# Kernel tuning notes

Hardware: AMD Instinct MI355X
Metric: run time of the kernel (lower is better)

Reference implementation:

```python
import jax, jax.numpy as jnp
import numpy as np

B, S, D, H, FF = 2, 2048, 1024, 16, 4096
HD = D // H          # head dim = 64
ROT = HD // 2        # rotary dim = dim/(num_heads*2) = 32 (partial rotation)
EPS = 1e-5


def setup_inputs() -> dict:
    key = jax.random.key(0)
    ks = jax.random.split(key, 16)
    std = 0.02
    return {
        "x": jax.random.normal(ks[0], (B, S, D), jnp.float32),
        "mask": jnp.ones((B, 1, 1, S), jnp.int32),
        "wq": jax.random.normal(ks[1], (D, D), jnp.float32) * std,
        "bq": jnp.zeros((D,), jnp.float32),
        "wk": jax.random.normal(ks[2], (D, D), jnp.float32) * std,
        "bk": jnp.zeros((D,), jnp.float32),
        "wv": jax.random.normal(ks[3], (D, D), jnp.float32) * std,
        "bv": jnp.zeros((D,), jnp.float32),
        "wo": jax.random.normal(ks[4], (D, D), jnp.float32) * std,
        "bo": jnp.zeros((D,), jnp.float32),
        "ln1_w": jnp.ones((D,), jnp.float32),
        "ln1_b": jnp.zeros((D,), jnp.float32),
        "ln2_w": jnp.ones((D,), jnp.float32),
        "ln2_b": jnp.zeros((D,), jnp.float32),
        "w1": jax.random.normal(ks[5], (D, FF), jnp.float32) * std,
        "b1": jnp.zeros((FF,), jnp.float32),
        "w2": jax.random.normal(ks[6], (FF, D), jnp.float32) * std,
        "b2": jnp.zeros((D,), jnp.float32),
    }


def _layernorm(x, w, b):
    mu = jnp.mean(x, axis=-1, keepdims=True)
    var = jnp.mean(jnp.square(x - mu), axis=-1, keepdims=True)
    return (x - mu) * jax.lax.rsqrt(var + EPS) * w + b


def _rope(t):
    # t: [B, H, S, HD]; rotate first ROT features, interleaved (GPT-J) pairing
    inv_freq = 1.0 / (10000.0 ** (jnp.arange(0, ROT, 2, dtype=jnp.float32) / ROT))
    ang = jnp.arange(S, dtype=jnp.float32)[:, None] * inv_freq      # [S, ROT//2]
    ang = jnp.repeat(ang, 2, axis=-1)                               # [S, ROT]
    cos, sin = jnp.cos(ang), jnp.sin(ang)
    t_rot, t_pass = t[..., :ROT], t[..., ROT:]
    pr = t_rot.reshape(*t_rot.shape[:-1], ROT // 2, 2)
    rot = jnp.stack([-pr[..., 1], pr[..., 0]], axis=-1).reshape(t_rot.shape)
    return jnp.concatenate([t_rot * cos + rot * sin, t_pass], axis=-1)


def reference(x, mask, wq, bq, wk, bk, wv, bv, wo, bo,
              ln1_w, ln1_b, ln2_w, ln2_b, w1, b1, w2, b2):
    res = x
    h = _layernorm(x, ln1_w, ln1_b)
    q = (h @ wq + bq).reshape(B, S, H, HD).transpose(0, 2, 1, 3)
    k = (h @ wk + bk).reshape(B, S, H, HD).transpose(0, 2, 1, 3)
    v = (h @ wv + bv).reshape(B, S, H, HD).transpose(0, 2, 1, 3)
    q, k = _rope(q), _rope(k)
    score = jnp.einsum('bhqd,bhkd->bhqk', q, k) * (1.0 / np.sqrt(HD))
    score = jnp.where(mask == 0, jnp.float32(-1e9), score)
    attn = jax.nn.softmax(score, axis=-1)
    out = jnp.einsum('bhqk,bhkd->bhqd', attn, v)
    out = out.transpose(0, 2, 1, 3).reshape(B, S, D) @ wo + bo
    x = res + out
    res = x
    h = _layernorm(x, ln2_w, ln2_b)
    h = jax.nn.gelu(h @ w1 + b1, approximate=False) @ w2 + b2
    return res + h
```

## Files before the change

kernel.cpp:

```cpp
#include <hip/hip_runtime.h>
#include <cstdint>
#include <cstddef>


typedef __bf16 bf16;
typedef __bf16 bf16x2 __attribute__((ext_vector_type(2)));
typedef __bf16 bf16x4v __attribute__((ext_vector_type(4)));
typedef __bf16 bf16x8 __attribute__((ext_vector_type(8)));
typedef float  f32x4  __attribute__((ext_vector_type(4)));

#define NB 2
#define NS 2048
#define ND 1024
#define NH 16
#define NHD 64
#define NFF 4096
#define NM (NB*NS)
#define QKSCALE 0.18033688011112042f

typedef uint32_t __attribute__((address_space(1))) gu32_t;
typedef uint32_t __attribute__((address_space(3))) lu32_t;
__device__ __forceinline__ void async_copy16(void* lds, const void* g) {
  __builtin_amdgcn_global_load_lds((gu32_t*)g, (lu32_t*)lds, 16, 0, 0);
}

__device__ __forceinline__ bf16x4v tr_read16(const void* p) {
  typedef const __attribute__((address_space(3))) unsigned char* lp;
  bf16x4v d;
  asm volatile("ds_read_b64_tr_b16 %0, %1" : "=v"(d) : "v"((lp)p));
  return d;
}

__device__ __forceinline__ float gelu_f(float x) {
  return 0.5f * x * (1.0f + erff(x * 0.70710678118654752f));
}

__global__ __launch_bounds__(256) void transpose_all(
    const float* __restrict__ wq, const float* __restrict__ wk,
    const float* __restrict__ wv, const float* __restrict__ wo,
    const float* __restrict__ w1, const float* __restrict__ w2,
    bf16* __restrict__ wqt, bf16* __restrict__ wkt, bf16* __restrict__ wvt,
    bf16* __restrict__ wot, bf16* __restrict__ w1t, bf16* __restrict__ w2t) {
  __shared__ float t[32][33];
  int flat = blockIdx.x;
  const float* W; bf16* Wt; long bx, by; int K, N;
  if (flat < 4096) {
    int which = flat >> 10, r = flat & 1023;
    const float* Ws[4] = {wq, wk, wv, wo};
    bf16* Wts[4] = {wqt, wkt, wvt, wot};
    W = Ws[which]; Wt = Wts[which]; bx = r & 31; by = r >> 5; K = ND; N = ND;
  } else if (flat < 8192) {
    int r = flat - 4096;
    W = w1; Wt = w1t; bx = r & 127; by = r >> 7; K = ND; N = NFF;
  } else {
    int r = flat - 8192;
    W = w2; Wt = w2t; bx = r & 31; by = r >> 5; K = NFF; N = ND;
  }
  int tx = threadIdx.x, ty = threadIdx.y;
#pragma unroll
  for (int r = 0; r < 4; ++r)
    t[ty + r*8][tx] = W[(by*32 + ty + r*8) * (long)N + bx*32 + tx];
  __syncthreads();
#pragma unroll
  for (int r = 0; r < 4; ++r)
    Wt[(bx*32 + ty + r*8) * (long)K + by*32 + tx] = (bf16)t[tx][ty + r*8];
}

__global__ __launch_bounds__(256) void smallfuse_kernel(
    const float* __restrict__ a, const float* __restrict__ b,
    const float* __restrict__ c, float* __restrict__ o,
    const int* __restrict__ mask, float* __restrict__ m01f,
    bf16* __restrict__ m01b, float2* __restrict__ rtab) {
  int blk = blockIdx.x;
  int t = threadIdx.x;
  if (blk < 12) {
    int i = blk * 256 + t;
    o[i] = (i < ND) ? a[i] : ((i < 2*ND) ? b[i - ND] : c[i - 2*ND]);
  } else if (blk < 28) {
    int i = (blk - 12) * 256 + t;
    float v = mask[i] ? 1.0f : 0.0f;
    m01f[i] = v;
    m01b[i] = (bf16)v;
  } else {
    int idx = (blk - 28) * 256 + t;
    int s = idx >> 4, i = idx & 15;
    float ang = (float)s * exp2f(-(float)i * (13.287712379549449f / 16.0f));
    float sn, cs;
    sincosf(ang, &sn, &cs);
    rtab[idx] = make_float2(cs, sn);
  }
}

__global__ __launch_bounds__(256) void ln_kernel(
    const float* __restrict__ x, const float* __restrict__ w,
    const float* __restrict__ b, bf16* __restrict__ out) {
  long row = blockIdx.x;
  int t = threadIdx.x;
  float4 v = ((const float4*)(x + row*ND))[t];
  float s  = v.x + v.y + v.z + v.w;
  float sq = v.x*v.x + v.y*v.y + v.z*v.z + v.w*v.w;
#pragma unroll
  for (int m = 1; m <= 32; m <<= 1) { s += __shfl_xor(s, m); sq += __shfl_xor(sq, m); }
  __shared__ float ss[4], ssq[4];
  if ((t & 63) == 0) { ss[t>>6] = s; ssq[t>>6] = sq; }
  __syncthreads();
  s  = ss[0] + ss[1] + ss[2] + ss[3];
  sq = ssq[0] + ssq[1] + ssq[2] + ssq[3];
  float mu = s * (1.0f/ND);
  float rs = rsqrtf(sq * (1.0f/ND) - mu*mu + 1e-5f);
  float4 wv = ((const float4*)w)[t];
  float4 bv = ((const float4*)b)[t];
  bf16x4v o;
  o[0] = (bf16)((v.x-mu)*rs*wv.x + bv.x);
  o[1] = (bf16)((v.y-mu)*rs*wv.y + bv.y);
  o[2] = (bf16)((v.z-mu)*rs*wv.z + bv.z);
  o[3] = (bf16)((v.w-mu)*rs*wv.w + bv.w);
  *(bf16x4v*)(out + row*ND + t*4) = o;
}

template<int EPI>
__global__ __launch_bounds__(512, 2) void gemm256_kernel(
    const bf16* __restrict__ A, const bf16* __restrict__ Bt,
    const float* __restrict__ bias, void* __restrict__ Cout,
    const float2* __restrict__ rtab, const float* __restrict__ m01f,
    int M, int N, int K) {
  __shared__ __align__(16) bf16 Alds[4][256*32];
  __shared__ __align__(16) bf16 Blds[4][256*32];
  const int tid = threadIdx.x, lane = tid & 63, w = tid >> 6;
  const int fr = lane & 15, kg = lane >> 4;
  const int wr = w >> 2, wc = w & 3;
  const int swb = (kg ^ ((fr >> 1) & 3)) << 4;

  const int gx = gridDim.x;
  int lin = blockIdx.y * gx + blockIdx.x;
  int nwg = gx * gridDim.y;
  int swz = (lin & 7) * (nwg >> 3) + (lin >> 3);
  const long am0 = (long)(swz / gx) * 256;
  const long bn0 = (long)(swz % gx) * 256;

  const f32x4 fzero = {0.f, 0.f, 0.f, 0.f};
  f32x4 acc[8][4];
#pragma unroll
  for (int m = 0; m < 8; ++m)
#pragma unroll
    for (int n = 0; n < 4; ++n) acc[m][n] = fzero;

  auto stage = [&](int kt, int bufi) {
#pragma unroll
    for (int i = 0; i < 2; ++i) {
      int s = i*512 + tid;
      int r = s >> 2, c = (s & 3) ^ ((s >> 3) & 3);
      async_copy16((char*)&Alds[bufi][0] + i*8192 + w*1024,
                   &A[(am0 + r)*K + kt + c*8]);
      async_copy16((char*)&Blds[bufi][0] + i*8192 + w*1024,
                   &Bt[(bn0 + r)*K + kt + c*8]);
    }
  };

  const int nk = K >> 5;
  stage(0, 0);
  stage(32, 1);
  asm volatile("s_waitcnt vmcnt(4)" ::: "memory");
  __builtin_amdgcn_s_barrier();
  __builtin_amdgcn_sched_barrier(0);

  for (int t = 0; t < nk; ++t) {
    const int cur = t & 3;
    if (t + 2 < nk) stage((t + 2) * 32, (t + 2) & 3);
    const char* Ab = (const char*)&Alds[cur][0];
    const char* Bb = (const char*)&Blds[cur][0];
    bf16x8 af[4], bfv[4];
#pragma unroll
    for (int n = 0; n < 4; ++n) bfv[n] = *(const bf16x8*)(Bb + (wc*64 + n*16 + fr)*64 + swb);
#pragma unroll
    for (int m = 0; m < 4; ++m) af[m]  = *(const bf16x8*)(Ab + (wr*128 + m*16 + fr)*64 + swb);
    asm volatile("s_waitcnt lgkmcnt(0)" ::: "memory");
    __builtin_amdgcn_sched_barrier(0);
    __builtin_amdgcn_s_setprio(1);
#pragma unroll
    for (int m = 0; m < 4; ++m)
#pragma unroll
      for (int n = 0; n < 4; ++n)
        acc[m][n] = __builtin_amdgcn_mfma_f32_16x16x32_bf16(af[m], bfv[n], acc[m][n], 0, 0, 0);
    __builtin_amdgcn_s_setprio(0);
    __builtin_amdgcn_s_barrier();
#pragma unroll
    for (int m = 0; m < 4; ++m) af[m] = *(const bf16x8*)(Ab + (wr*128 + (m+4)*16 + fr)*64 + swb);
    asm volatile("s_waitcnt lgkmcnt(0)" ::: "memory");
    __builtin_amdgcn_sched_barrier(0);
    __builtin_amdgcn_s_setprio(1);
#pragma unroll
    for (int m = 0; m < 4; ++m)
#pragma unroll
      for (int n = 0; n < 4; ++n)
        acc[m+4][n] = __builtin_amdgcn_mfma_f32_16x16x32_bf16(af[m], bfv[n], acc[m+4][n], 0, 0, 0);
    __builtin_amdgcn_s_setprio(0);
    if (t + 2 < nk) { asm volatile("s_waitcnt vmcnt(4)" ::: "memory"); }
    else            { asm volatile("s_waitcnt vmcnt(0)" ::: "memory"); }
    __builtin_amdgcn_s_barrier();
    __builtin_amdgcn_sched_barrier(0);
  }

  const int rbase = kg * 4;
  const int region = (int)(bn0 >> 10);
#pragma unroll
  for (int m = 0; m < 8; ++m) {
#pragma unroll
    for (int n = 0; n < 4; ++n) {
      long col = bn0 + wc*64 + n*16 + fr;
      float bia = bias[col];
#pragma unroll
      for (int j = 0; j < 4; ++j) {
        long row = am0 + wr*128 + m*16 + rbase + j;
        float val = acc[m][n][j] + bia;
        if (EPI == 1) {
          ((bf16*)Cout)[row * N + col] = (bf16)gelu_f(val);
        } else {
          if (region <= 1) {
            float pval = __shfl_xor(val, 1);
            if (n < 2) {
              float2 cs = rtab[((row & (NS-1)) << 4) | ((n*16 + fr) >> 1)];
              val = (fr & 1) ? val*cs.x + pval*cs.y : val*cs.x - pval*cs.y;
            }
            if (region == 0) val *= QKSCALE;
          } else {
            val *= m01f[row];
          }
          ((bf16*)Cout)[(long)region * (NM*(long)ND) + row * ND + (col & 1023)] = (bf16)val;
        }
      }
    }
  }
}

__global__ __launch_bounds__(512, 1) void gemm128x8_kernel(
    const bf16* __restrict__ A, const bf16* __restrict__ Bt,
    const float* __restrict__ bias, const float* __restrict__ res,
    float* __restrict__ Cout, int M, int N, int K) {
  __shared__ __align__(16) bf16 Alds[4][128*64];
  __shared__ __align__(16) bf16 Blds[4][128*64];
  const int tid = threadIdx.x, lane = tid & 63, w = tid >> 6;
  const int fr = lane & 15, kg = lane >> 4;
  const int wr = w >> 1, wc = w & 1;

  const int gx = gridDim.x;
  int lin = blockIdx.y * gx + blockIdx.x;
  int nwg = gx * gridDim.y;
  int swz = (lin & 7) * (nwg >> 3) + (lin >> 3);
  const long am0 = (long)(swz / gx) * 128;
  const long bn0 = (long)(swz % gx) * 128;

  const f32x4 fzero = {0.f, 0.f, 0.f, 0.f};
  f32x4 acc[2][4];
#pragma unroll
  for (int m = 0; m < 2; ++m)
#pragma unroll
    for (int n = 0; n < 4; ++n) acc[m][n] = fzero;

  auto stage = [&](int kt, int bufi) {
#pragma unroll
    for (int i = 0; i < 2; ++i) {
      int s = i*512 + tid;
      int r = s >> 3, c = (s & 7) ^ (r & 7);
      async_copy16((char*)&Alds[bufi][0] + i*8192 + w*1024,
                   &A[(am0 + r)*K + kt + c*8]);
      async_copy16((char*)&Blds[bufi][0] + i*8192 + w*1024,
                   &Bt[(bn0 + r)*K + kt + c*8]);
    }
  };

  const int nk = K >> 6;
  stage(0, 0);
  stage(64, 1);
  asm volatile("s_waitcnt vmcnt(4)" ::: "memory");
  __builtin_amdgcn_s_barrier();
  __builtin_amdgcn_sched_barrier(0);

  for (int t = 0; t < nk; ++t) {
    const int cur = t & 3;
    if (t + 2 < nk) stage((t + 2) * 64, (t + 2) & 3);
    const char* Ab = (const char*)&Alds[cur][0];
    const char* Bb = (const char*)&Blds[cur][0];
    bf16x8 af[2][2], bfv[2][4];
#pragma unroll
    for (int kk = 0; kk < 2; ++kk) {
#pragma unroll
      for (int m = 0; m < 2; ++m) {
        int r = wr*32 + m*16 + fr;
        af[kk][m] = *(const bf16x8*)(Ab + r*128 + (((kk*4 + kg) ^ (r & 7)) << 4));
      }
#pragma unroll
      for (int n = 0; n < 4; ++n) {
        int r = wc*64 + n*16 + fr;
        bfv[kk][n] = *(const bf16x8*)(Bb + r*128 + (((kk*4 + kg) ^ (r & 7)) << 4));
      }
    }
    asm volatile("s_waitcnt lgkmcnt(0)" ::: "memory");
    __builtin_amdgcn_sched_barrier(0);
    __builtin_amdgcn_s_setprio(1);
#pragma unroll
    for (int kk = 0; kk < 2; ++kk)
#pragma unroll
      for (int m = 0; m < 2; ++m)
#pragma unroll
        for (int n = 0; n < 4; ++n)
          acc[m][n] = __builtin_amdgcn_mfma_f32_16x16x32_bf16(af[kk][m], bfv[kk][n], acc[m][n], 0, 0, 0);
    __builtin_amdgcn_s_setprio(0);
    if (t + 2 < nk) { asm volatile("s_waitcnt vmcnt(4)" ::: "memory"); }
    else            { asm volatile("s_waitcnt vmcnt(0)" ::: "memory"); }
    __builtin_amdgcn_s_barrier();
    __builtin_amdgcn_sched_barrier(0);
  }

  const int rbase = kg * 4;
#pragma unroll
  for (int m = 0; m < 2; ++m) {
#pragma unroll
    for (int n = 0; n < 4; ++n) {
      long col = bn0 + wc*64 + n*16 + fr;
      float bia = bias[col];
#pragma unroll
      for (int j = 0; j < 4; ++j) {
        long row = am0 + wr*32 + m*16 + rbase + j;
        Cout[row * N + col] = acc[m][n][j] + bia + res[row * N + col];
      }
    }
  }
}

__global__ __launch_bounds__(256) void attn_kernel(
    const bf16* __restrict__ q, const bf16* __restrict__ k,
    const bf16* __restrict__ v, const bf16* __restrict__ m01b,
    bf16* __restrict__ out) {
  int lin = blockIdx.y * 32 + blockIdx.x;
  int swz = (lin & 7) * 128 + (lin >> 3);
  const int qt = swz & 31;
  const int b = swz >> 9, h = (swz >> 5) & 15;
  const int tid = threadIdx.x, lane = tid & 63, w = tid >> 6;
  const int fr = lane & 15, kg = lane >> 4;
  const int k8 = kg * 8;
  const int frl = fr & 3, frh = fr >> 2;

  __shared__ __align__(16) bf16 Klds[2][64*64];
  __shared__ __align__(16) bf16 Vlds[2][64*64];

  const long qrow = (long)qt*64 + w*16 + fr;
  const bf16* qbase = q + ((long)b*NS + qrow)*ND + h*NHD;
  bf16x8 qf[2];
  qf[0] = *(const bf16x8*)(qbase + k8);
  qf[1] = *(const bf16x8*)(qbase + 32 + k8);

  const bf16* kbase = k + (long)b*NS*ND + h*NHD;
  const bf16* vbase = v + (long)b*NS*ND + h*NHD;
  const bf16* mbase = m01b + (long)b*NS;

  auto stageK = [&](int kt, int bufi) {
#pragma unroll
    for (int i = 0; i < 2; ++i) {
      int slot = i*256 + tid;
      int row = slot >> 3, c = slot & 7;
      int csrc = c ^ (row & 7) ^ (((row >> 3) & 1) << 2);
      async_copy16((char*)&Klds[bufi][0] + i*4096 + w*1024,
                   kbase + ((long)kt*64 + row)*ND + csrc*8);
    }
  };
  auto stageV = [&](int kt, int bufi) {
#pragma unroll
    for (int i = 0; i < 2; ++i) {
      int kr = i*32 + (tid >> 5)*4 + ((tid & 7) >> 1);
      int dc = ((tid >> 3) & 3)*16 + (tid & 1)*8;
      async_copy16((char*)&Vlds[bufi][0] + i*4096 + w*1024,
                   vbase + ((long)kt*64 + kr)*ND + dc);
    }
  };

  const f32x4 fzero = {0.f, 0.f, 0.f, 0.f};
  f32x4 oacc[4], oaccL = fzero;
#pragma unroll
  for (int n = 0; n < 4; ++n) oacc[n] = fzero;

  stageK(0, 0);
  stageV(0, 0);
  asm volatile("s_waitcnt vmcnt(0)" ::: "memory");
  __builtin_amdgcn_s_barrier();
  __builtin_amdgcn_sched_barrier(0);

  const int NT = NS / 64;
  for (int kt = 0; kt < NT; ++kt) {
    const int cur = kt & 1;
    if (kt + 1 < NT) { stageK(kt + 1, cur ^ 1); stageV(kt + 1, cur ^ 1); }
    bf16x8 vbm[2];
    vbm[0] = *(const bf16x8*)(mbase + kt*64 + k8);
    vbm[1] = *(const bf16x8*)(mbase + kt*64 + 32 + k8);
    const char* Kb = (const char*)&Klds[cur][0];
    const char* Vb = (const char*)&Vlds[cur][0];

    f32x4 sacc[4];
#pragma unroll
    for (int n = 0; n < 4; ++n) sacc[n] = fzero;
#pragma unroll
    for (int n = 0; n < 4; ++n) {
      int r = (frh << 3) + ((n & 1) << 2) + frl + ((n >> 1) << 5);
      int swzr = (r & 7) ^ (((r >> 3) & 1) << 2);
#pragma unroll
      for (int kk = 0; kk < 2; ++kk) {
        bf16x8 kf = *(const bf16x8*)(Kb + r*128 + ((((kk << 2) | kg) ^ swzr) << 4));
        sacc[n] = __builtin_amdgcn_mfma_f32_16x16x32_bf16(kf, qf[kk], sacc[n], 0, 0, 0);
      }
    }

    float p[4][4];
#pragma unroll
    for (int n = 0; n < 4; ++n) {
      p[n][0] = exp2f(sacc[n][0]);
      p[n][1] = exp2f(sacc[n][1]);
      p[n][2] = exp2f(sacc[n][2]);
      p[n][3] = exp2f(sacc[n][3]);
    }

    bf16x8 paf[2];
#pragma unroll
    for (int n = 0; n < 4; ++n) {
#pragma unroll
      for (int j = 0; j < 4; ++j)
        paf[n >> 1][((n & 1) << 2) + j] = (bf16)p[n][j];
    }

    oaccL = __builtin_amdgcn_mfma_f32_16x16x32_bf16(paf[0], vbm[0], oaccL, 0, 0, 0);
    oaccL = __builtin_amdgcn_mfma_f32_16x16x32_bf16(paf[1], vbm[1], oaccL, 0, 0, 0);

#pragma unroll
    for (int kk = 0; kk < 2; ++kk) {
      bf16x4v t0[4], t1[4];
#pragma unroll
      for (int n2 = 0; n2 < 4; ++n2) {
        t0[n2] = tr_read16(Vb + (((kk*8 + 0)*4 + n2)*128 + kg*1024 + fr*8));
        t1[n2] = tr_read16(Vb + (((kk*8 + 1)*4 + n2)*128 + kg*1024 + fr*8));
      }
      asm volatile("s_waitcnt lgkmcnt(0)" ::: "memory");
      __builtin_amdgcn_sched_barrier(0);
#pragma unroll
      for (int n2 = 0; n2 < 4; ++n2) {
        bf16x8 vb8 = __builtin_shufflevector(t0[n2], t1[n2], 0, 1, 2, 3, 4, 5, 6, 7);
        oacc[n2] = __builtin_amdgcn_mfma_f32_16x16x32_bf16(paf[kk], vb8, oacc[n2], 0, 0, 0);
      }
    }

    asm volatile("s_waitcnt vmcnt(0)" ::: "memory");
    __builtin_amdgcn_s_barrier();
    __builtin_amdgcn_sched_barrier(0);
  }

#pragma unroll
  for (int j = 0; j < 4; ++j) {
    float inv = 1.0f / oaccL[j];
    long orow = (long)qt*64 + w*16 + kg*4 + j;
    bf16* ob = out + ((long)b*NS + orow)*ND + h*NHD;
#pragma unroll
    for (int n2 = 0; n2 < 4; ++n2) ob[n2*16 + fr] = (bf16)(oacc[n2][j] * inv);
  }
}

extern "C" void kernel_launch(void* const* d_in, const int* in_sizes, int n_in,
                              void* d_out, int out_size, void* d_ws, size_t ws_size,
                              hipStream_t stream) {
  const float* x    = (const float*)d_in[0];
  const int*   mask = (const int*)d_in[1];
  const float* wq   = (const float*)d_in[2];
  const float* bq   = (const float*)d_in[3];
  const float* wk   = (const float*)d_in[4];
  const float* bk   = (const float*)d_in[5];
  const float* wv   = (const float*)d_in[6];
  const float* bv   = (const float*)d_in[7];
  const float* wo   = (const float*)d_in[8];
  const float* bo   = (const float*)d_in[9];
  const float* ln1w = (const float*)d_in[10];
  const float* ln1b = (const float*)d_in[11];
  const float* ln2w = (const float*)d_in[12];
  const float* ln2b = (const float*)d_in[13];
  const float* w1   = (const float*)d_in[14];
  const float* b1   = (const float*)d_in[15];
  const float* w2   = (const float*)d_in[16];
  const float* b2   = (const float*)d_in[17];
  float* out = (float*)d_out;

  char* ws = (char*)d_ws;
  const size_t MB = 1024ull * 1024ull;
  bf16* wqt = (bf16*)(ws + 0*MB);
  bf16* wkt = (bf16*)(ws + 2*MB);
  bf16* wvt = (bf16*)(ws + 4*MB);
  bf16* wot = (bf16*)(ws + 6*MB);
  bf16* w1t = (bf16*)(ws + 8*MB);
  bf16* w2t = (bf16*)(ws + 16*MB);
  bf16* h1   = (bf16*)(ws + 24*MB);
  bf16* qb   = (bf16*)(ws + 32*MB);
  bf16* kb   = (bf16*)(ws + 40*MB);
  bf16* vb   = (bf16*)(ws + 48*MB);
  bf16* attn = h1;
  bf16* f1   = (bf16*)(ws + 24*MB);
  float* y1  = (float*)(ws + 56*MB);
  bf16* h2   = (bf16*)(ws + 72*MB);
  float* bcat = (float*)(ws + 80*MB);
  float* m01f = (float*)(ws + 80*MB + 16*1024);
  bf16*  m01b = (bf16*) (ws + 80*MB + 32*1024);
  float2* rtab = (float2*)(ws + 80*MB + 48*1024);
  (void)in_sizes; (void)n_in; (void)out_size; (void)ws_size;

  transpose_all<<<12288, dim3(32, 8), 0, stream>>>(wq, wk, wv, wo, w1, w2,
                                                   wqt, wkt, wvt, wot, w1t, w2t);
  smallfuse_kernel<<<156, 256, 0, stream>>>(bq, bk, bv, bcat, mask, m01f, m01b, rtab);

  ln_kernel<<<NM, 256, 0, stream>>>(x, ln1w, ln1b, h1);

  gemm256_kernel<3><<<dim3(12, 16), 512, 0, stream>>>(h1, wqt, bcat, qb,
                                                      rtab, m01f, NM, 3*ND, ND);
  attn_kernel<<<dim3(NS/64, NB*NH), 256, 0, stream>>>(qb, kb, vb, m01b, attn);

  gemm128x8_kernel<<<dim3(8, 32), 512, 0, stream>>>(attn, wot, bo, x, y1,
                                                    NM, ND, ND);
  ln_kernel<<<NM, 256, 0, stream>>>(y1, ln2w, ln2b, h2);
  gemm256_kernel<1><<<dim3(16, 16), 512, 0, stream>>>(h2, w1t, b1, f1,
                                                      nullptr, nullptr, NM, NFF, ND);
  gemm128x8_kernel<<<dim3(8, 32), 512, 0, stream>>>(f1, w2t, b2, y1, out,
                                                    NM, ND, NFF);
}
```

Before: 297.0 us.

## Merge prep kernels, pre-transpose V, triple-buffer attention with 128-row tiles

Folds the weight transpose, small setup work and the first layernorm into one prep kernel, removing two launches. The QKV GEMM epilogue now writes V transposed per head so attention can read V fragments with plain vector LDS loads instead of transpose reads. The attention kernel moves to 512 threads covering 128 query rows, triple-buffers K/V in LDS with a two-tile prefetch, and stages the mask in LDS. The price is more LDS per block, scattered strided writes of V in the GEMM epilogue, and a large merged prep grid.

```diff
diff --git a/kernel.cpp b/kernel.cpp
--- a/kernel.cpp
+++ b/kernel.cpp
@@ -24,70 +24,87 @@
   __builtin_amdgcn_global_load_lds((gu32_t*)g, (lu32_t*)lds, 16, 0, 0);
 }
 
-__device__ __forceinline__ bf16x4v tr_read16(const void* p) {
-  typedef const __attribute__((address_space(3))) unsigned char* lp;
-  bf16x4v d;
-  asm volatile("ds_read_b64_tr_b16 %0, %1" : "=v"(d) : "v"((lp)p));
-  return d;
-}
-
 __device__ __forceinline__ float gelu_f(float x) {
   return 0.5f * x * (1.0f + erff(x * 0.70710678118654752f));
 }
 
-__global__ __launch_bounds__(256) void transpose_all(
+__global__ __launch_bounds__(256) void prep_kernel(
     const float* __restrict__ wq, const float* __restrict__ wk,
     const float* __restrict__ wv, const float* __restrict__ wo,
     const float* __restrict__ w1, const float* __restrict__ w2,
     bf16* __restrict__ wqt, bf16* __restrict__ wkt, bf16* __restrict__ wvt,
-    bf16* __restrict__ wot, bf16* __restrict__ w1t, bf16* __restrict__ w2t) {
-  __shared__ float t[32][33];
+    bf16* __restrict__ wot, bf16* __restrict__ w1t, bf16* __restrict__ w2t,
+    const float* __restrict__ bq, const float* __restrict__ bk,
+    const float* __restrict__ bv, float* __restrict__ bcat,
+    const int* __restrict__ mask, float* __restrict__ m01f,
+    bf16* __restrict__ m01b, float2* __restrict__ rtab,
+    const float* __restrict__ x, const float* __restrict__ ln1w,
+    const float* __restrict__ ln1b, bf16* __restrict__ h1) {
   int flat = blockIdx.x;
-  const float* W; bf16* Wt; long bx, by; int K, N;
-  if (flat < 4096) {
-    int which = flat >> 10, r = flat & 1023;
-    const float* Ws[4] = {wq, wk, wv, wo};
-    bf16* Wts[4] = {wqt, wkt, wvt, wot};
-    W = Ws[which]; Wt = Wts[which]; bx = r & 31; by = r >> 5; K = ND; N = ND;
-  } else if (flat < 8192) {
-    int r = flat - 4096;
-    W = w1; Wt = w1t; bx = r & 127; by = r >> 7; K = ND; N = NFF;
+  int t = threadIdx.x;
+  if (flat < 12288) {
+    __shared__ float tile[32][33];
+    const float* W; bf16* Wt; long bx, by; int K, N;
+    if (flat < 4096) {
+      int which = flat >> 10, r = flat & 1023;
+      const float* Ws[4] = {wq, wk, wv, wo};
+      bf16* Wts[4] = {wqt, wkt, wvt, wot};
+      W = Ws[which]; Wt = Wts[which]; bx = r & 31; by = r >> 5; K = ND; N = ND;
+    } else if (flat < 8192) {
+      int r = flat - 4096;
+      W = w1; Wt = w1t; bx = r & 127; by = r >> 7; K = ND; N = NFF;
+    } else {
+      int r = flat - 8192;
+      W = w2; Wt = w2t; bx = r & 31; by = r >> 5; K = NFF; N = ND;
+    }
+    int tx = t & 31, ty = t >> 5;
+#pragma unroll
+    for (int r = 0; r < 4; ++r)
+      tile[ty + r*8][tx] = W[(by*32 + ty + r*8) * (long)N + bx*32 + tx];
+    __syncthreads();
+#pragma unroll
+    for (int r = 0; r < 4; ++r)
+      Wt[(bx*32 + ty + r*8) * (long)K + by*32 + tx] = (bf16)tile[tx][ty + r*8];
+  } else if (flat < 12444) {
+    int blk = flat - 12288;
+    if (blk < 12) {
+      int i = blk * 256 + t;
+      bcat[i] = (i < ND) ? bq[i] : ((i < 2*ND) ? bk[i - ND] : bv[i - 2*ND]);
+    } else if (blk < 28) {
+      int i = (blk - 12) * 256 + t;
+      float v = mask[i] ? 1.0f : 0.0f;
+      m01f[i] = v;
+      m01b[i] = (bf16)v;
+    } else {
+      int idx = (blk - 28) * 256 + t;
+      int s = idx >> 4, i = idx & 15;
+      float ang = (float)s * exp2f(-(float)i * (13.287712379549449f / 16.0f));
+      float sn, cs;
+      sincosf(ang, &sn, &cs);
+      rtab[idx] = make_float2(cs, sn);
+    }
   } else {
-    int r = flat - 8192;
-    W = w2; Wt = w2t; bx = r & 31; by = r >> 5; K = NFF; N = ND;
-  }
-  int tx = threadIdx.x, ty = threadIdx.y;
-#pragma unroll
-  for (int r = 0; r < 4; ++r)
-    t[ty + r*8][tx] = W[(by*32 + ty + r*8) * (long)N + bx*32 + tx];
-  __syncthreads();
-#pragma unroll
-  for (int r = 0; r < 4; ++r)
-    Wt[(bx*32 + ty + r*8) * (long)K + by*32 + tx] = (bf16)t[tx][ty + r*8];
-}
-
-__global__ __launch_bounds__(256) void smallfuse_kernel(
-    const float* __restrict__ a, const float* __restrict__ b,
-    const float* __restrict__ c, float* __restrict__ o,
-    const int* __restrict__ mask, float* __restrict__ m01f,
-    bf16* __restrict__ m01b, float2* __restrict__ rtab) {
-  int blk = blockIdx.x;
-  int t = threadIdx.x;
-  if (blk < 12) {
-    int i = blk * 256 + t;
-    o[i] = (i < ND) ? a[i] : ((i < 2*ND) ? b[i - ND] : c[i - 2*ND]);
-  } else if (blk < 28) {
-    int i = (blk - 12) * 256 + t;
-    float v = mask[i] ? 1.0f : 0.0f;
-    m01f[i] = v;
-    m01b[i] = (bf16)v;
-  } else {
-    int idx = (blk - 28) * 256 + t;
-    int s = idx >> 4, i = idx & 15;
-    float ang = (float)s * exp2f(-(float)i * (13.287712379549449f / 16.0f));
-    float sn, cs;
-    sincosf(ang, &sn, &cs);
-    rtab[idx] = make_float2(cs, sn);
+    long row = flat - 12444;
+    float4 v = ((const float4*)(x + row*ND))[t];
+    float s  = v.x + v.y + v.z + v.w;
+    float sq = v.x*v.x + v.y*v.y + v.z*v.z + v.w*v.w;
+#pragma unroll
+    for (int m = 1; m <= 32; m <<= 1) { s += __shfl_xor(s, m); sq += __shfl_xor(sq, m); }
+    __shared__ float ss[4], ssq[4];
+    if ((t & 63) == 0) { ss[t>>6] = s; ssq[t>>6] = sq; }
+    __syncthreads();
+    s  = ss[0] + ss[1] + ss[2] + ss[3];
+    sq = ssq[0] + ssq[1] + ssq[2] + ssq[3];
+    float mu = s * (1.0f/ND);
+    float rs = rsqrtf(sq * (1.0f/ND) - mu*mu + 1e-5f);
+    float4 wv4 = ((const float4*)ln1w)[t];
+    float4 bv4 = ((const float4*)ln1b)[t];
+    bf16x4v o;
+    o[0] = (bf16)((v.x-mu)*rs*wv4.x + bv4.x);
+    o[1] = (bf16)((v.y-mu)*rs*wv4.y + bv4.y);
+    o[2] = (bf16)((v.z-mu)*rs*wv4.z + bv4.z);
+    o[3] = (bf16)((v.w-mu)*rs*wv4.w + bv4.w);
+    *(bf16x4v*)(h1 + row*ND + t*4) = o;
   }
 }
 
@@ -216,6 +233,7 @@
         if (EPI == 1) {
           ((bf16*)Cout)[row * N + col] = (bf16)gelu_f(val);
         } else {
+          long cv = col & 1023;
           if (region <= 1) {
             float pval = __shfl_xor(val, 1);
             if (n < 2) {
@@ -223,10 +241,12 @@
               val = (fr & 1) ? val*cs.x + pval*cs.y : val*cs.x - pval*cs.y;
             }
             if (region == 0) val *= QKSCALE;
+            ((bf16*)Cout)[(long)region * (NM*(long)ND) + row * ND + cv] = (bf16)val;
           } else {
             val *= m01f[row];
+            long vidx = (((row >> 11) << 4) | (cv >> 6)) * (64L*NS) + (cv & 63) * (long)NS + (row & 2047);
+            ((bf16*)Cout)[2L * NM * ND + vidx] = (bf16)val;
           }
-          ((bf16*)Cout)[(long)region * (NM*(long)ND) + row * ND + (col & 1023)] = (bf16)val;
         }
       }
     }
@@ -328,50 +348,46 @@
   }
 }
 
-__global__ __launch_bounds__(256) void attn_kernel(
+__global__ __launch_bounds__(512) void attn_kernel(
     const bf16* __restrict__ q, const bf16* __restrict__ k,
-    const bf16* __restrict__ v, const bf16* __restrict__ m01b,
+    const bf16* __restrict__ vt, const bf16* __restrict__ m01b,
     bf16* __restrict__ out) {
-  int lin = blockIdx.y * 32 + blockIdx.x;
-  int swz = (lin & 7) * 128 + (lin >> 3);
-  const int qt = swz & 31;
-  const int b = swz >> 9, h = (swz >> 5) & 15;
+  int lin = blockIdx.y * 16 + blockIdx.x;
+  int swz = (lin & 7) * 64 + (lin >> 3);
+  const int qt = swz & 15;
+  const int bh = swz >> 4;
+  const int b = bh >> 4, h = bh & 15;
   const int tid = threadIdx.x, lane = tid & 63, w = tid >> 6;
   const int fr = lane & 15, kg = lane >> 4;
   const int k8 = kg * 8;
   const int frl = fr & 3, frh = fr >> 2;
 
-  __shared__ __align__(16) bf16 Klds[2][64*64];
-  __shared__ __align__(16) bf16 Vlds[2][64*64];
-
-  const long qrow = (long)qt*64 + w*16 + fr;
+  __shared__ __align__(16) bf16 Klds[3][64*64];
+  __shared__ __align__(16) bf16 Vlds[3][64*64];
+  __shared__ __align__(16) bf16 Mlds[NS];
+
+  const long qrow = (long)qt*128 + w*16 + fr;
   const bf16* qbase = q + ((long)b*NS + qrow)*ND + h*NHD;
   bf16x8 qf[2];
   qf[0] = *(const bf16x8*)(qbase + k8);
   qf[1] = *(const bf16x8*)(qbase + 32 + k8);
 
   const bf16* kbase = k + (long)b*NS*ND + h*NHD;
-  const bf16* vbase = v + (long)b*NS*ND + h*NHD;
+  const bf16* vtb = vt + (long)bh*64*NS;
   const bf16* mbase = m01b + (long)b*NS;
 
+  if (w < 4) async_copy16((char*)Mlds + w*1024, mbase + tid*8);
+
+  const int srow = tid >> 3, sc = tid & 7;
+  const int csK = (sc ^ (srow & 7) ^ (((srow >> 3) & 1) << 2));
+  const int csV = (sc ^ (srow & 7));
   auto stageK = [&](int kt, int bufi) {
-#pragma unroll
-    for (int i = 0; i < 2; ++i) {
-      int slot = i*256 + tid;
-      int row = slot >> 3, c = slot & 7;
-      int csrc = c ^ (row & 7) ^ (((row >> 3) & 1) << 2);
-      async_copy16((char*)&Klds[bufi][0] + i*4096 + w*1024,
-                   kbase + ((long)kt*64 + row)*ND + csrc*8);
-    }
+    async_copy16((char*)&Klds[bufi][0] + w*1024,
+                 kbase + ((long)kt*64 + srow)*ND + csK*8);
   };
   auto stageV = [&](int kt, int bufi) {
-#pragma unroll
-    for (int i = 0; i < 2; ++i) {
-      int kr = i*32 + (tid >> 5)*4 + ((tid & 7) >> 1);
-      int dc = ((tid >> 3) & 3)*16 + (tid & 1)*8;
-      async_copy16((char*)&Vlds[bufi][0] + i*4096 + w*1024,
-                   vbase + ((long)kt*64 + kr)*ND + dc);
-    }
+    async_copy16((char*)&Vlds[bufi][0] + w*1024,
+                 vtb + (long)srow*NS + kt*64 + csV*8);
   };
 
   const f32x4 fzero = {0.f, 0.f, 0.f, 0.f};
@@ -379,21 +395,25 @@
 #pragma unroll
   for (int n = 0; n < 4; ++n) oacc[n] = fzero;
 
-  stageK(0, 0);
-  stageV(0, 0);
-  asm volatile("s_waitcnt vmcnt(0)" ::: "memory");
+  stageK(0, 0); stageV(0, 0);
+  stageK(1, 1); stageV(1, 1);
+  asm volatile("s_waitcnt vmcnt(2)" ::: "memory");
   __builtin_amdgcn_s_barrier();
   __builtin_amdgcn_sched_barrier(0);
 
   const int NT = NS / 64;
+  int bcur = 0, bpre = 1;
   for (int kt = 0; kt < NT; ++kt) {
-    const int cur = kt & 1;
-    if (kt + 1 < NT) { stageK(kt + 1, cur ^ 1); stageV(kt + 1, cur ^ 1); }
-    bf16x8 vbm[2];
-    vbm[0] = *(const bf16x8*)(mbase + kt*64 + k8);
-    vbm[1] = *(const bf16x8*)(mbase + kt*64 + 32 + k8);
-    const char* Kb = (const char*)&Klds[cur][0];
-    const char* Vb = (const char*)&Vlds[cur][0];
+    if (kt + 2 < NT) {
+      bpre = (bpre == 2) ? 0 : bpre + 1;
+      stageK(kt + 2, bpre);
+      stageV(kt + 2, bpre);
+    }
+    const char* Kb = (const char*)&Klds[bcur][0];
+    const char* Vb = (const char*)&Vlds[bcur][0];
+
+    bf16x8 vbm0 = *(const bf16x8*)&Mlds[kt*64 + k8];
+    bf16x8 vbm1 = *(const bf16x8*)&Mlds[kt*64 + 32 + k8];
 
     f32x4 sacc[4];
 #pragma unroll
@@ -426,35 +446,30 @@
         paf[n >> 1][((n & 1) << 2) + j] = (bf16)p[n][j];
     }
 
-    oaccL = __builtin_amdgcn_mfma_f32_16x16x32_bf16(paf[0], vbm[0], oaccL, 0, 0, 0);
-    oaccL = __builtin_amdgcn_mfma_f32_16x16x32_bf16(paf[1], vbm[1], oaccL, 0, 0, 0);
+    oaccL = __builtin_amdgcn_mfma_f32_16x16x32_bf16(paf[0], vbm0, oaccL, 0, 0, 0);
+    oaccL = __builtin_amdgcn_mfma_f32_16x16x32_bf16(paf[1], vbm1, oaccL, 0, 0, 0);
 
 #pragma unroll
     for (int kk = 0; kk < 2; ++kk) {
-      bf16x4v t0[4], t1[4];
 #pragma unroll
       for (int n2 = 0; n2 < 4; ++n2) {
-        t0[n2] = tr_read16(Vb + (((kk*8 + 0)*4 + n2)*128 + kg*1024 + fr*8));
-        t1[n2] = tr_read16(Vb + (((kk*8 + 1)*4 + n2)*128 + kg*1024 + fr*8));
-      }
-      asm volatile("s_waitcnt lgkmcnt(0)" ::: "memory");
-      __builtin_amdgcn_sched_barrier(0);
-#pragma unroll
-      for (int n2 = 0; n2 < 4; ++n2) {
-        bf16x8 vb8 = __builtin_shufflevector(t0[n2], t1[n2], 0, 1, 2, 3, 4, 5, 6, 7);
+        int r = n2*16 + fr;
+        bf16x8 vb8 = *(const bf16x8*)(Vb + r*128 + ((((kk << 2) | kg) ^ (r & 7)) << 4));
         oacc[n2] = __builtin_amdgcn_mfma_f32_16x16x32_bf16(paf[kk], vb8, oacc[n2], 0, 0, 0);
       }
     }
 
-    asm volatile("s_waitcnt vmcnt(0)" ::: "memory");
+    if (kt + 2 < NT)      { asm volatile("s_waitcnt vmcnt(2)" ::: "memory"); }
+    else if (kt + 1 < NT) { asm volatile("s_waitcnt vmcnt(0)" ::: "memory"); }
     __builtin_amdgcn_s_barrier();
     __builtin_amdgcn_sched_barrier(0);
+    bcur = (bcur == 2) ? 0 : bcur + 1;
   }
 
 #pragma unroll
   for (int j = 0; j < 4; ++j) {
     float inv = 1.0f / oaccL[j];
-    long orow = (long)qt*64 + w*16 + kg*4 + j;
+    long orow = (long)qt*128 + w*16 + kg*4 + j;
     bf16* ob = out + ((long)b*NS + orow)*ND + h*NHD;
 #pragma unroll
     for (int n2 = 0; n2 < 4; ++n2) ob[n2*16 + fr] = (bf16)(oacc[n2][j] * inv);
@@ -495,7 +510,7 @@
   bf16* h1   = (bf16*)(ws + 24*MB);
   bf16* qb   = (bf16*)(ws + 32*MB);
   bf16* kb   = (bf16*)(ws + 40*MB);
-  bf16* vb   = (bf16*)(ws + 48*MB);
+  bf16* vtb  = (bf16*)(ws + 48*MB);
   bf16* attn = h1;
   bf16* f1   = (bf16*)(ws + 24*MB);
   float* y1  = (float*)(ws + 56*MB);
@@ -506,15 +521,14 @@
   float2* rtab = (float2*)(ws + 80*MB + 48*1024);
   (void)in_sizes; (void)n_in; (void)out_size; (void)ws_size;
 
-  transpose_all<<<12288, dim3(32, 8), 0, stream>>>(wq, wk, wv, wo, w1, w2,
-                                                   wqt, wkt, wvt, wot, w1t, w2t);
-  smallfuse_kernel<<<156, 256, 0, stream>>>(bq, bk, bv, bcat, mask, m01f, m01b, rtab);
-
-  ln_kernel<<<NM, 256, 0, stream>>>(x, ln1w, ln1b, h1);
+  prep_kernel<<<16540, 256, 0, stream>>>(wq, wk, wv, wo, w1, w2,
+                                         wqt, wkt, wvt, wot, w1t, w2t,
+                                         bq, bk, bv, bcat, mask, m01f, m01b,
+                                         rtab, x, ln1w, ln1b, h1);
 
   gemm256_kernel<3><<<dim3(12, 16), 512, 0, stream>>>(h1, wqt, bcat, qb,
                                                       rtab, m01f, NM, 3*ND, ND);
-  attn_kernel<<<dim3(NS/64, NB*NH), 256, 0, stream>>>(qb, kb, vb, m01b, attn);
+  attn_kernel<<<dim3(16, 32), 512, 0, stream>>>(qb, kb, vtb, m01b, attn);
 
   gemm128x8_kernel<<<dim3(8, 32), 512, 0, stream>>>(attn, wot, bo, x, y1,
                                                     NM, ND, ND);
```

Measured after the change: 308.3 us. 1.04x slower.
